# Performance work log

Measured on AMD Instinct MI355X. Metric: run time of the kernel, lower is better.

Reference implementation:

```python
import jax, jax.numpy as jnp
import numpy as np
from jax import lax

B, C_IN, C_OUT, H, W, K, PAD = 4, 64, 64, 96, 96, 3, 1
K2 = K * K


def setup_inputs() -> dict:
    key = jax.random.key(0)
    k1, k2, k3, k4, k5 = jax.random.split(key, 5)
    x = jax.random.normal(k1, (B, C_IN, H, W), jnp.float32)
    offset = jax.random.normal(k2, (B, 2 * K2, H, W), jnp.float32)
    weight = jax.random.normal(k3, (C_OUT, C_IN, K, K), jnp.float32) * 0.05
    mask_weight = jax.random.normal(k4, (K2, C_IN, K, K), jnp.float32) * 0.05
    mask_bias = jax.random.normal(k5, (K2,), jnp.float32) * 0.05
    return {"x": x, "offset": offset, "weight": weight,
            "mask_weight": mask_weight, "mask_bias": mask_bias}


def _deform_conv2d(x, offset, weight, mask):
    # torchvision ordering: per kernel tap k, offset[:, 2k] is dy, offset[:, 2k+1] is dx
    off_y = offset[:, 0::2]  # [B, K2, H, W]
    off_x = offset[:, 1::2]
    ky, kx = jnp.meshgrid(jnp.arange(K), jnp.arange(K), indexing="ij")
    ky = ky.reshape(K2).astype(x.dtype)
    kx = kx.reshape(K2).astype(x.dtype)
    hh = jnp.arange(H, dtype=x.dtype)
    ww = jnp.arange(W, dtype=x.dtype)
    base_y = hh[None, :, None] - PAD + ky[:, None, None]   # [K2, H, 1]
    base_x = ww[None, None, :] - PAD + kx[:, None, None]   # [K2, 1, W]
    py = base_y[None] + off_y                               # [B, K2, H, W]
    px = base_x[None] + off_x

    y0 = jnp.floor(py)
    x0 = jnp.floor(px)
    wy = py - y0   # bilinear weights
    wx = px - x0
    y0i = y0.astype(jnp.int32)
    x0i = x0.astype(jnp.int32)

    x_flat = x.reshape(B, C_IN, H * W)

    def gather(yy, xx):
        valid = (yy >= 0) & (yy < H) & (xx >= 0) & (xx < W)
        idx = jnp.clip(yy, 0, H - 1) * W + jnp.clip(xx, 0, W - 1)  # [B,K2,H,W]
        idx_f = idx.reshape(B, -1)
        v = jax.vmap(lambda xf, i: xf[:, i])(x_flat, idx_f)  # [B, C, K2*H*W]
        v = v.reshape(B, C_IN, K2, H, W)
        return v * valid[:, None].astype(v.dtype)

    v00 = gather(y0i, x0i)
    v01 = gather(y0i, x0i + 1)
    v10 = gather(y0i + 1, x0i)
    v11 = gather(y0i + 1, x0i + 1)

    wy_ = wy[:, None]  # [B,1,K2,H,W]
    wx_ = wx[:, None]
    sampled = (v00 * (1 - wy_) * (1 - wx_) + v01 * (1 - wy_) * wx_
               + v10 * wy_ * (1 - wx_) + v11 * wy_ * wx_)
    sampled = sampled * mask[:, None]  # modulate by sigmoid mask

    w2 = weight.reshape(C_OUT, C_IN, K2)
    return jnp.einsum("bckhw,ock->bohw", sampled, w2)


def reference(x, offset, weight, mask_weight, mask_bias):
    mask_logits = lax.conv_general_dilated(
        x, mask_weight, window_strides=(1, 1), padding=[(PAD, PAD), (PAD, PAD)],
        dimension_numbers=("NCHW", "OIHW", "NCHW"))
    mask = jax.nn.sigmoid(mask_logits + mask_bias[None, :, None, None])
    return _deform_conv2d(x, offset, weight, mask)
```

## Files before the change

### kernel.cpp

```cpp
#include <hip/hip_runtime.h>
#include <math.h>

#define BB 4
#define CI 64
#define CO 64
#define HH 96
#define WW 96
#define HW (HH*WW)
#define K2 9
#define NT (HW/64)
#define PADC 1

typedef __attribute__((ext_vector_type(8))) short short8;
typedef __attribute__((ext_vector_type(4))) float float4v;

#define XT_USHORTS ((size_t)BB*HW*64)
#define WF_USHORTS (18*64*32)
#define MWF_USHORTS (18*16*32)

__device__ __forceinline__ float bf2f(short s) {
    return __uint_as_float(((unsigned int)(unsigned short)s) << 16);
}
__device__ __forceinline__ short f2bf(float f) {
    unsigned int u = __float_as_uint(f);
    u = (u + 0x7fffu + ((u >> 16) & 1u)) >> 16;
    return (short)u;
}

__global__ __launch_bounds__(256) void xt_kernel(const float* __restrict__ x,
                                                 unsigned short* __restrict__ xT) {
    __shared__ unsigned short tile[64][72];
    int t = threadIdx.x, bid = blockIdx.x;
    int b = bid / NT, p0 = (bid % NT) * 64;
    int px = t & 63, cg = t >> 6;
    const float* xb = x + (size_t)b * CI * HW + p0;
    #pragma unroll
    for (int i = 0; i < 16; i++) {
        int c = cg * 16 + i;
        tile[px][c] = (unsigned short)f2bf(xb[(size_t)c * HW + px]);
    }
    __syncthreads();
    int c = t & 63, pg = t >> 6;
    unsigned short* xo = xT + ((size_t)b * HW + p0) * 64;
    #pragma unroll
    for (int i = 0; i < 16; i++) {
        int pp = pg * 16 + i;
        xo[(size_t)pp * 64 + c] = tile[pp][c];
    }
}

__global__ __launch_bounds__(256) void pack_kernel(const float* __restrict__ wgt,
                                                   const float* __restrict__ mw,
                                                   unsigned short* __restrict__ Wf,
                                                   unsigned short* __restrict__ MWf) {
    int i = blockIdx.x * 256 + threadIdx.x;
    if (i < WF_USHORTS) {
        int frag = i >> 11;
        int o = (i >> 5) & 63;
        int tt = i & 31;
        int k = frag >> 1, cc = frag & 1;
        int c = cc * 32 + tt;
        Wf[i] = (unsigned short)f2bf(wgt[o * 576 + c * 9 + k]);
    } else if (i < WF_USHORTS + MWF_USHORTS) {
        int e = i - WF_USHORTS;
        int frag = e >> 9;
        int m = (e >> 5) & 15;
        int tt = e & 31;
        int q = frag >> 1, cc = frag & 1;
        int c = cc * 32 + tt;
        MWf[e] = (m < 9) ? (unsigned short)f2bf(mw[m * 576 + c * 9 + q]) : 0;
    }
}

__global__ __launch_bounds__(256) void fused_kernel(const float* __restrict__ off,
                                                    const float* __restrict__ mbias,
                                                    const unsigned short* __restrict__ xT,
                                                    const unsigned short* __restrict__ Wf,
                                                    const unsigned short* __restrict__ MWf,
                                                    float* __restrict__ out) {
    __shared__ float s_mask[K2][64];
    __shared__ int   s_idx[K2][4][64];
    __shared__ float s_w[K2][4][64];

    int t = threadIdx.x;
    int lane = t & 63, wv = t >> 6;
    int n = lane & 15, quad = lane >> 4;
    int b = blockIdx.x / NT;
    int p0 = (blockIdx.x % NT) * 64;
    int pxl = wv * 16 + n;
    int p = p0 + pxl;
    int h = p / WW, wc = p % WW;
    const unsigned short* xTb = xT + (size_t)b * HW * 64;

    {
        float4v acc = {0.f, 0.f, 0.f, 0.f};
        #pragma unroll
        for (int q = 0; q < 9; q++) {
            int hh = h + q / 3 - 1, ww2 = wc + q % 3 - 1;
            bool valid = (hh >= 0) && (hh < HH) && (ww2 >= 0) && (ww2 < WW);
            int nidx = valid ? (hh * WW + ww2) : 0;
            const unsigned short* src = xTb + (size_t)nidx * 64 + quad * 8;
            #pragma unroll
            for (int cc = 0; cc < 2; cc++) {
                short8 bfrag = {0, 0, 0, 0, 0, 0, 0, 0};
                if (valid) bfrag = *(const short8*)(src + cc * 32);
                short8 afrag = *(const short8*)(MWf + ((size_t)((q * 2 + cc) * 16 + n)) * 32 + quad * 8);
                acc = __builtin_amdgcn_mfma_f32_16x16x32_bf16(afrag, bfrag, acc, 0, 0, 0);
            }
        }
        #pragma unroll
        for (int r = 0; r < 4; r++) {
            int row = quad * 4 + r;
            if (row < 9) {
                float s = acc[r] + mbias[row];
                s_mask[row][pxl] = 1.f / (1.f + expf(-s));
            }
        }
    }
    __syncthreads();

    for (int e = t; e < K2 * 64; e += 256) {
        int k = e >> 6, pe = e & 63;
        int pp = p0 + pe;
        int hh0 = pp / WW, ww0 = pp % WW;
        int ky = k / 3, kx = k % 3;
        float oy = off[((size_t)b * 2 * K2 + 2 * k) * HW + pp];
        float ox = off[((size_t)b * 2 * K2 + 2 * k + 1) * HW + pp];
        float m = s_mask[k][pe];
        float py = (float)(hh0 - PADC + ky) + oy;
        float pxf = (float)(ww0 - PADC + kx) + ox;
        float y0f = floorf(py), x0f = floorf(pxf);
        float wy = py - y0f, wx = pxf - x0f;
        int y0 = (int)y0f, x0 = (int)x0f;
        int y1 = y0 + 1, x1 = x0 + 1;
        int y0c = min(max(y0, 0), HH - 1), y1c = min(max(y1, 0), HH - 1);
        int x0c = min(max(x0, 0), WW - 1), x1c = min(max(x1, 0), WW - 1);
        bool vy0 = (y0 >= 0) && (y0 < HH), vy1 = (y1 >= 0) && (y1 < HH);
        bool vx0 = (x0 >= 0) && (x0 < WW), vx1 = (x1 >= 0) && (x1 < WW);
        float w00 = (1.f - wy) * (1.f - wx) * m; if (!(vy0 && vx0)) w00 = 0.f;
        float w01 = (1.f - wy) * wx * m;         if (!(vy0 && vx1)) w01 = 0.f;
        float w10 = wy * (1.f - wx) * m;         if (!(vy1 && vx0)) w10 = 0.f;
        float w11 = wy * wx * m;                 if (!(vy1 && vx1)) w11 = 0.f;
        s_idx[k][0][pe] = y0c * WW + x0c;
        s_idx[k][1][pe] = y0c * WW + x1c;
        s_idx[k][2][pe] = y1c * WW + x0c;
        s_idx[k][3][pe] = y1c * WW + x1c;
        s_w[k][0][pe] = w00; s_w[k][1][pe] = w01;
        s_w[k][2][pe] = w10; s_w[k][3][pe] = w11;
    }
    __syncthreads();

    float4v acc0 = {0.f, 0.f, 0.f, 0.f};
    float4v acc1 = {0.f, 0.f, 0.f, 0.f};
    float4v acc2 = {0.f, 0.f, 0.f, 0.f};
    float4v acc3 = {0.f, 0.f, 0.f, 0.f};

    for (int k = 0; k < 9; k++) {
        int i0 = s_idx[k][0][pxl], i1 = s_idx[k][1][pxl];
        int i2 = s_idx[k][2][pxl], i3 = s_idx[k][3][pxl];
        float w0 = s_w[k][0][pxl], w1 = s_w[k][1][pxl];
        float w2 = s_w[k][2][pxl], w3 = s_w[k][3][pxl];
        #pragma unroll
        for (int cc = 0; cc < 2; cc++) {
            int co = cc * 32 + quad * 8;
            short8 u0 = *(const short8*)(xTb + (size_t)i0 * 64 + co);
            short8 u1 = *(const short8*)(xTb + (size_t)i1 * 64 + co);
            short8 u2 = *(const short8*)(xTb + (size_t)i2 * 64 + co);
            short8 u3 = *(const short8*)(xTb + (size_t)i3 * 64 + co);
            short8 bfrag;
            #pragma unroll
            for (int j = 0; j < 8; j++) {
                float v = bf2f(u0[j]) * w0 + bf2f(u1[j]) * w1 +
                          bf2f(u2[j]) * w2 + bf2f(u3[j]) * w3;
                bfrag[j] = f2bf(v);
            }
            const unsigned short* wp = Wf + (size_t)((k * 2 + cc) * 64) * 32 + quad * 8;
            short8 a0 = *(const short8*)(wp + (0 * 16 + n) * 32);
            short8 a1 = *(const short8*)(wp + (1 * 16 + n) * 32);
            short8 a2 = *(const short8*)(wp + (2 * 16 + n) * 32);
            short8 a3 = *(const short8*)(wp + (3 * 16 + n) * 32);
            acc0 = __builtin_amdgcn_mfma_f32_16x16x32_bf16(a0, bfrag, acc0, 0, 0, 0);
            acc1 = __builtin_amdgcn_mfma_f32_16x16x32_bf16(a1, bfrag, acc1, 0, 0, 0);
            acc2 = __builtin_amdgcn_mfma_f32_16x16x32_bf16(a2, bfrag, acc2, 0, 0, 0);
            acc3 = __builtin_amdgcn_mfma_f32_16x16x32_bf16(a3, bfrag, acc3, 0, 0, 0);
        }
    }

    float* ob = out + (size_t)b * CO * HW + p0 + pxl;
    #pragma unroll
    for (int r = 0; r < 4; r++) {
        ob[(size_t)(0 * 16 + quad * 4 + r) * HW] = acc0[r];
        ob[(size_t)(1 * 16 + quad * 4 + r) * HW] = acc1[r];
        ob[(size_t)(2 * 16 + quad * 4 + r) * HW] = acc2[r];
        ob[(size_t)(3 * 16 + quad * 4 + r) * HW] = acc3[r];
    }
}

extern "C" void kernel_launch(void* const* d_in, const int* in_sizes, int n_in,
                              void* d_out, int out_size, void* d_ws, size_t ws_size,
                              hipStream_t stream) {
    const float* x   = (const float*)d_in[0];
    const float* off = (const float*)d_in[1];
    const float* wgt = (const float*)d_in[2];
    const float* mw  = (const float*)d_in[3];
    const float* mb  = (const float*)d_in[4];
    float* out = (float*)d_out;

    unsigned short* xT  = (unsigned short*)d_ws;
    unsigned short* Wf  = xT + XT_USHORTS;
    unsigned short* MWf = Wf + WF_USHORTS;

    hipLaunchKernelGGL(xt_kernel, dim3(BB * NT), dim3(256), 0, stream, x, xT);
    hipLaunchKernelGGL(pack_kernel, dim3((WF_USHORTS + MWF_USHORTS + 255) / 256), dim3(256),
                       0, stream, wgt, mw, Wf, MWf);
    hipLaunchKernelGGL(fused_kernel, dim3(BB * NT), dim3(256), 0, stream,
                       off, mb, xT, Wf, MWf, out);
}
```

Measured before the change: 122.0 us.

## Prefetch bilinear gathers two taps ahead, swizzle block order, vectorize transpose

The main loop now holds a two-deep register buffer and issues the eight gather loads for tap k+2 while tap k is interpolated and fed to MFMA, so gather latency is hidden. Blocks are remapped so consecutive block IDs cycle across batches and two tile halves, which changes L2 locality and load spread. The transpose kernel now uses float4 global reads and 16-byte writes. The prefetch raises VGPR use, which may lower occupancy.

```diff
diff --git a/kernel.cpp b/kernel.cpp
--- a/kernel.cpp
+++ b/kernel.cpp
@@ -27,26 +27,36 @@
     return (short)u;
 }
 
+__device__ __forceinline__ void unswz(int bid, int* b, int* tile) {
+    int g = bid & 7, r = bid >> 3;
+    *b = g & 3;
+    *tile = (g >> 2) * 72 + r;
+}
+
 __global__ __launch_bounds__(256) void xt_kernel(const float* __restrict__ x,
                                                  unsigned short* __restrict__ xT) {
-    __shared__ unsigned short tile[64][72];
-    int t = threadIdx.x, bid = blockIdx.x;
-    int b = bid / NT, p0 = (bid % NT) * 64;
-    int px = t & 63, cg = t >> 6;
+    __shared__ unsigned short ts[64][72];
+    int t = threadIdx.x;
+    int b, tl; unswz(blockIdx.x, &b, &tl);
+    int p0 = tl * 64;
     const float* xb = x + (size_t)b * CI * HW + p0;
+    int pq = t & 15, cg = t >> 4;
     #pragma unroll
-    for (int i = 0; i < 16; i++) {
-        int c = cg * 16 + i;
-        tile[px][c] = (unsigned short)f2bf(xb[(size_t)c * HW + px]);
+    for (int i = 0; i < 4; i++) {
+        int c = cg + i * 16;
+        float4v v = *(const float4v*)(xb + (size_t)c * HW + pq * 4);
+        ts[pq * 4 + 0][c] = (unsigned short)f2bf(v[0]);
+        ts[pq * 4 + 1][c] = (unsigned short)f2bf(v[1]);
+        ts[pq * 4 + 2][c] = (unsigned short)f2bf(v[2]);
+        ts[pq * 4 + 3][c] = (unsigned short)f2bf(v[3]);
     }
     __syncthreads();
-    int c = t & 63, pg = t >> 6;
-    unsigned short* xo = xT + ((size_t)b * HW + p0) * 64;
-    #pragma unroll
-    for (int i = 0; i < 16; i++) {
-        int pp = pg * 16 + i;
-        xo[(size_t)pp * 64 + c] = tile[pp][c];
-    }
+    int px = t >> 2, cq = t & 3;
+    unsigned short* xo = xT + ((size_t)b * HW + p0 + px) * 64 + cq * 16;
+    short8 v0 = *(const short8*)&ts[px][cq * 16];
+    short8 v1 = *(const short8*)&ts[px][cq * 16 + 8];
+    *(short8*)xo = v0;
+    *(short8*)(xo + 8) = v1;
 }
 
 __global__ __launch_bounds__(256) void pack_kernel(const float* __restrict__ wgt,
@@ -85,8 +95,8 @@
     int t = threadIdx.x;
     int lane = t & 63, wv = t >> 6;
     int n = lane & 15, quad = lane >> 4;
-    int b = blockIdx.x / NT;
-    int p0 = (blockIdx.x % NT) * 64;
+    int b, tl; unswz(blockIdx.x, &b, &tl);
+    int p0 = tl * 64;
     int pxl = wv * 16 + n;
     int p = p0 + pxl;
     int h = p / WW, wc = p % WW;
@@ -155,23 +165,40 @@
     float4v acc2 = {0.f, 0.f, 0.f, 0.f};
     float4v acc3 = {0.f, 0.f, 0.f, 0.f};
 
-    for (int k = 0; k < 9; k++) {
+    const unsigned short* xq = xTb + quad * 8;
+    short8 st[2][8];
+
+    auto loadK = [&](int k, short8* dst) {
         int i0 = s_idx[k][0][pxl], i1 = s_idx[k][1][pxl];
         int i2 = s_idx[k][2][pxl], i3 = s_idx[k][3][pxl];
+        dst[0] = *(const short8*)(xq + (size_t)i0 * 64);
+        dst[1] = *(const short8*)(xq + (size_t)i0 * 64 + 32);
+        dst[2] = *(const short8*)(xq + (size_t)i1 * 64);
+        dst[3] = *(const short8*)(xq + (size_t)i1 * 64 + 32);
+        dst[4] = *(const short8*)(xq + (size_t)i2 * 64);
+        dst[5] = *(const short8*)(xq + (size_t)i2 * 64 + 32);
+        dst[6] = *(const short8*)(xq + (size_t)i3 * 64);
+        dst[7] = *(const short8*)(xq + (size_t)i3 * 64 + 32);
+    };
+
+    loadK(0, st[0]);
+    loadK(1, st[1]);
+
+    #pragma unroll
+    for (int k = 0; k < 9; k++) {
         float w0 = s_w[k][0][pxl], w1 = s_w[k][1][pxl];
         float w2 = s_w[k][2][pxl], w3 = s_w[k][3][pxl];
+        short8 cur[8];
+        #pragma unroll
+        for (int j = 0; j < 8; j++) cur[j] = st[k & 1][j];
+        if (k + 2 < 9) loadK(k + 2, st[k & 1]);
         #pragma unroll
         for (int cc = 0; cc < 2; cc++) {
-            int co = cc * 32 + quad * 8;
-            short8 u0 = *(const short8*)(xTb + (size_t)i0 * 64 + co);
-            short8 u1 = *(const short8*)(xTb + (size_t)i1 * 64 + co);
-            short8 u2 = *(const short8*)(xTb + (size_t)i2 * 64 + co);
-            short8 u3 = *(const short8*)(xTb + (size_t)i3 * 64 + co);
             short8 bfrag;
             #pragma unroll
             for (int j = 0; j < 8; j++) {
-                float v = bf2f(u0[j]) * w0 + bf2f(u1[j]) * w1 +
-                          bf2f(u2[j]) * w2 + bf2f(u3[j]) * w3;
+                float v = bf2f(cur[cc][j])     * w0 + bf2f(cur[2 + cc][j]) * w1 +
+                          bf2f(cur[4 + cc][j]) * w2 + bf2f(cur[6 + cc][j]) * w3;
                 bfrag[j] = f2bf(v);
             }
             const unsigned short* wp = Wf + (size_t)((k * 2 + cc) * 64) * 32 + quad * 8;
```

After: 122.2 us. Within noise of the previous version (+0.1%).
